# Performance work log

Hardware: AMD Instinct MI355X
Metric: run time of the kernel (lower is better)

Reference implementation:

```python
import jax, jax.numpy as jnp
import numpy as np

A = 2048        # atoms
IN_DEPTH = 128
OUT_DEPTH = 128
FILTER_LEN = 16


def setup_inputs() -> dict:
    key = jax.random.key(0)
    k1, k2, k3, k4 = jax.random.split(key, 4)
    node_property_tensor = jax.random.normal(k1, (A, IN_DEPTH), dtype=jnp.float32)
    connectivity_tensor = jax.random.normal(k2, (A, A, FILTER_LEN), dtype=jnp.float32)
    bond_property_tensor = jax.random.normal(k3, (A, FILTER_LEN, 2), dtype=jnp.float32)
    # filters initialized ~ N(0,1) * 1/in_depth, per the torch init
    filters = jax.random.normal(k4, (OUT_DEPTH, FILTER_LEN, IN_DEPTH + 2), dtype=jnp.float32) / IN_DEPTH
    return {
        "node_property_tensor": node_property_tensor,
        "connectivity_tensor": connectivity_tensor,
        "bond_property_tensor": bond_property_tensor,
        "filters": filters,
    }


def reference(node_property_tensor, connectivity_tensor, bond_property_tensor, filters):
    # gather neighbor features: conn (A,B,F) x node (B,D) -> (A,F,D)
    node_connection = jnp.einsum('abf,bd->afd', connectivity_tensor, node_property_tensor)
    # append bond properties -> (A, F, D+2)
    combined = jnp.concatenate([node_connection, bond_property_tensor], axis=2)
    # fused broadcast-multiply + double-sum: (A,F,K) x (O,F,K) -> (A,O)
    return jnp.einsum('afk,ofk->ao', combined, filters)
```

## Files before the change

### kernel.cpp

```cpp
#include <hip/hip_runtime.h>
#include <stdint.h>

#define N_ATOM 2048
#define K_TOT  32768
#define KCH    2048
#define BK2    128
#define NIT    (KCH / BK2)

typedef __attribute__((ext_vector_type(8))) short bf16x8;
typedef __attribute__((ext_vector_type(4))) float f32x4;

typedef __attribute__((address_space(3))) uint32_t lds_u32;
typedef __attribute__((address_space(1))) uint32_t gbl_u32;

__device__ __forceinline__ void async_ld16(const void* g, void* l) {
  __builtin_amdgcn_global_load_lds((const gbl_u32*)g, (lds_u32*)l, 16, 0, 0);
}

__device__ __forceinline__ unsigned short f2bf(float x) {
  union { float f; uint32_t u; } v; v.f = x;
  uint32_t r = v.u + 0x7FFFu + ((v.u >> 16) & 1u);
  return (unsigned short)(r >> 16);
}

__global__ __launch_bounds__(256) void k_gt(const float* __restrict__ node,
                                            const float* __restrict__ filt,
                                            unsigned short* __restrict__ Gt) {
  __shared__ unsigned short As[128 * 136];
  __shared__ unsigned short Bs[128 * 136];
  const int t  = threadIdx.x;
  const int b0 = blockIdx.x * 128;
  const int n0 = blockIdx.y * 128;

#pragma unroll
  for (int rep = 0; rep < 16; ++rep) {
    int q = rep * 256 + t;
    int row = q >> 5, c4 = q & 31;
    float4 v = *(const float4*)(node + (size_t)(b0 + row) * 128 + c4 * 4);
    unsigned short* dst = &As[row * 136 + c4 * 4];
    dst[0] = f2bf(v.x); dst[1] = f2bf(v.y); dst[2] = f2bf(v.z); dst[3] = f2bf(v.w);
  }
#pragma unroll
  for (int rep = 0; rep < 32; ++rep) {
    int q = rep * 256 + t;
    int row = q >> 6, c2 = q & 63;
    float2 v = *(const float2*)(filt + (size_t)(n0 + row) * 130 + c2 * 2);
    unsigned short* dst = &Bs[row * 136 + c2 * 2];
    dst[0] = f2bf(v.x); dst[1] = f2bf(v.y);
  }
  __syncthreads();

  const int w = t >> 6, l = t & 63;
  const int lm = l & 15, q4 = l >> 4;

  f32x4 acc[2][8];
#pragma unroll
  for (int ms = 0; ms < 2; ++ms)
#pragma unroll
    for (int ns = 0; ns < 8; ++ns)
      acc[ms][ns] = (f32x4){0.f, 0.f, 0.f, 0.f};

#pragma unroll
  for (int ks = 0; ks < 4; ++ks) {
    int ko = ks * 32 + q4 * 8;
    bf16x8 a[2], b[8];
#pragma unroll
    for (int ms = 0; ms < 2; ++ms) {
      int m = w * 32 + ms * 16 + lm;
      a[ms] = *(const bf16x8*)&As[m * 136 + ko];
    }
#pragma unroll
    for (int ns = 0; ns < 8; ++ns) {
      int n = ns * 16 + lm;
      b[ns] = *(const bf16x8*)&Bs[n * 136 + ko];
    }
#pragma unroll
    for (int ms = 0; ms < 2; ++ms)
#pragma unroll
      for (int ns = 0; ns < 8; ++ns)
        acc[ms][ns] = __builtin_amdgcn_mfma_f32_16x16x32_bf16(a[ms], b[ns], acc[ms][ns], 0, 0, 0);
  }

#pragma unroll
  for (int ms = 0; ms < 2; ++ms)
#pragma unroll
    for (int ns = 0; ns < 8; ++ns)
#pragma unroll
      for (int i = 0; i < 4; ++i) {
        int m = w * 32 + ms * 16 + q4 * 4 + i;
        int n = ns * 16 + lm;
        Gt[(size_t)(b0 + m) * 2048 + n0 + n] = f2bf(acc[ms][ns][i]);
      }
}

__global__ __launch_bounds__(256) void k_bond(const float* __restrict__ bond,
                                              const float* __restrict__ filt,
                                              float* __restrict__ out) {
  __shared__ float fb[128 * 32];
  __shared__ float bl[16 * 32];
  const int t  = threadIdx.x;
  const int a0 = blockIdx.x * 16;

#pragma unroll
  for (int r = 0; r < 16; ++r) {
    int idx = r * 256 + t;
    int o = idx >> 5, fj = idx & 31;
    int f = fj >> 1, j = fj & 1;
    fb[idx] = filt[(size_t)o * 2080 + f * 130 + 128 + j];
  }
  bl[t]       = bond[(size_t)a0 * 32 + t];
  bl[256 + t] = bond[(size_t)a0 * 32 + 256 + t];
  __syncthreads();

#pragma unroll
  for (int r = 0; r < 8; ++r) {
    int idx = r * 256 + t;
    int aa = idx >> 7, o = idx & 127;
    const float2* bp = (const float2*)&bl[aa * 32];
    const float2* fp = (const float2*)&fb[o * 32];
    float acc = 0.f;
#pragma unroll
    for (int f = 0; f < 16; ++f) {
      float2 b2 = bp[f], f2 = fp[f];
      acc += b2.x * f2.x + b2.y * f2.y;
    }
    out[(size_t)(a0 + aa) * 128 + o] = acc;
  }
}

__global__ __launch_bounds__(256, 1) void k_main(const float* __restrict__ conn,
                                                 const unsigned short* __restrict__ Gt,
                                                 float* __restrict__ out) {
  __shared__ unsigned short Bh[2][8 * 128 * 16];

  const int t  = threadIdx.x;
  const int w  = t >> 6, l = t & 63;
  const int lm = l & 15, q4 = l >> 4;
  const int a0 = blockIdx.x * 128;
  const int kc = blockIdx.y * KCH;

  f32x4 acc[2][8];
#pragma unroll
  for (int ms = 0; ms < 2; ++ms)
#pragma unroll
    for (int ns = 0; ns < 8; ++ns)
      acc[ms][ns] = (f32x4){0.f, 0.f, 0.f, 0.f};

  const float* arow0 = conn + (size_t)(a0 + w * 32 + lm) * K_TOT;
  const float* arow1 = conn + (size_t)(a0 + w * 32 + 16 + lm) * K_TOT;

  auto stageB = [&](int buf, int k0) {
    const char* gB = (const char*)(Gt + (size_t)k0 * 128);
#pragma unroll
    for (int r = 0; r < 8; ++r) {
      const void* g = gB + (size_t)(r * 256 + t) * 16;
      void* lb = (void*)((char*)&Bh[buf][0] + r * 4096 + w * 1024);
      async_ld16(g, lb);
    }
  };

  float4 Ar[2][4][2];
  auto loadA = [&](int k0) {
#pragma unroll
    for (int kk = 0; kk < 4; ++kk) {
      int off = k0 + kk * 32 + q4 * 8;
      Ar[0][kk][0] = *(const float4*)(arow0 + off);
      Ar[0][kk][1] = *(const float4*)(arow0 + off + 4);
      Ar[1][kk][0] = *(const float4*)(arow1 + off);
      Ar[1][kk][1] = *(const float4*)(arow1 + off + 4);
    }
  };

  stageB(0, kc);
  loadA(kc);
  __syncthreads();

  for (int it = 0; it < NIT; ++it) {
    const int cur = it & 1;

    bf16x8 af[2][4];
#pragma unroll
    for (int ms = 0; ms < 2; ++ms)
#pragma unroll
      for (int kk = 0; kk < 4; ++kk) {
        float4 lo = Ar[ms][kk][0], hi = Ar[ms][kk][1];
        bf16x8 av;
        av[0] = (short)f2bf(lo.x); av[1] = (short)f2bf(lo.y);
        av[2] = (short)f2bf(lo.z); av[3] = (short)f2bf(lo.w);
        av[4] = (short)f2bf(hi.x); av[5] = (short)f2bf(hi.y);
        av[6] = (short)f2bf(hi.z); av[7] = (short)f2bf(hi.w);
        af[ms][kk] = av;
      }

    if (it + 1 < NIT) {
      stageB(1 - cur, kc + (it + 1) * BK2);
      loadA(kc + (it + 1) * BK2);
    }

#pragma unroll
    for (int kk = 0; kk < 4; ++kk) {
      const int b_rel = 2 * kk + (q4 >> 1);
      const int f0 = (q4 & 1) * 8;
      bf16x8 b[8];
#pragma unroll
      for (int ns = 0; ns < 8; ++ns) {
        int o = ns * 16 + lm;
        b[ns] = *(const bf16x8*)&Bh[cur][b_rel * 2048 + o * 16 + f0];
      }
#pragma unroll
      for (int ms = 0; ms < 2; ++ms)
#pragma unroll
        for (int ns = 0; ns < 8; ++ns)
          acc[ms][ns] = __builtin_amdgcn_mfma_f32_16x16x32_bf16(af[ms][kk], b[ns], acc[ms][ns], 0, 0, 0);
    }

    __syncthreads();
  }

#pragma unroll
  for (int ms = 0; ms < 2; ++ms)
#pragma unroll
    for (int ns = 0; ns < 8; ++ns)
#pragma unroll
      for (int i = 0; i < 4; ++i) {
        int m = w * 32 + ms * 16 + q4 * 4 + i;
        int n = ns * 16 + lm;
        atomicAdd(&out[(size_t)(a0 + m) * 128 + n], acc[ms][ns][i]);
      }
}

extern "C" void kernel_launch(void* const* d_in, const int* in_sizes, int n_in,
                              void* d_out, int out_size, void* d_ws, size_t ws_size,
                              hipStream_t stream) {
  const float* node = (const float*)d_in[0];
  const float* conn = (const float*)d_in[1];
  const float* bond = (const float*)d_in[2];
  const float* filt = (const float*)d_in[3];
  float* out = (float*)d_out;

  if (ws_size < (size_t)N_ATOM * 2048 * sizeof(unsigned short)) return;
  unsigned short* Gt = (unsigned short*)d_ws;

  k_gt  <<<dim3(16, 16), 256, 0, stream>>>(node, filt, Gt);
  k_bond<<<dim3(128),    256, 0, stream>>>(bond, filt, out);
  k_main<<<dim3(16, 16), 256, 0, stream>>>(conn, Gt, out);
}
```

Baseline: 430.0 us.

## Double waves per block in main GEMM, halve rows per wave, cheaper bf16 pack

Reorganizes the main GEMM kernel to use 8 waves per block, each owning 16 rows instead of 32, with launch bounds allowing two blocks per CU. This raises the number of waves in flight and lowers per-thread register use, to better hide latency on the streamed connectivity loads. It also switches those loads to nontemporal and replaces per-element bf16 rounding with a pack-and-permute conversion that drops the round-to-even tie term. The trade-off is less B-fragment reuse per LDS read and slightly different rounding.

```diff
diff --git a/kernel.cpp b/kernel.cpp
--- a/kernel.cpp
+++ b/kernel.cpp
@@ -21,6 +21,14 @@
   union { float f; uint32_t u; } v; v.f = x;
   uint32_t r = v.u + 0x7FFFu + ((v.u >> 16) & 1u);
   return (unsigned short)(r >> 16);
+}
+
+__device__ __forceinline__ uint32_t pack_bf2(float x, float y) {
+  union { float f; uint32_t u; } a, b;
+  a.f = x; b.f = y;
+  uint32_t au = a.u + 0x7FFFu;
+  uint32_t bu = b.u + 0x7FFFu;
+  return __builtin_amdgcn_perm(bu, au, 0x07060302u);
 }
 
 __global__ __launch_bounds__(256) void k_gt(const float* __restrict__ node,
@@ -128,7 +136,7 @@
   }
 }
 
-__global__ __launch_bounds__(256, 1) void k_main(const float* __restrict__ conn,
+__global__ __launch_bounds__(512, 2) void k_main(const float* __restrict__ conn,
                                                  const unsigned short* __restrict__ Gt,
                                                  float* __restrict__ out) {
   __shared__ unsigned short Bh[2][8 * 128 * 16];
@@ -139,35 +147,30 @@
   const int a0 = blockIdx.x * 128;
   const int kc = blockIdx.y * KCH;
 
-  f32x4 acc[2][8];
-#pragma unroll
-  for (int ms = 0; ms < 2; ++ms)
-#pragma unroll
-    for (int ns = 0; ns < 8; ++ns)
-      acc[ms][ns] = (f32x4){0.f, 0.f, 0.f, 0.f};
-
-  const float* arow0 = conn + (size_t)(a0 + w * 32 + lm) * K_TOT;
-  const float* arow1 = conn + (size_t)(a0 + w * 32 + 16 + lm) * K_TOT;
+  f32x4 acc[8];
+#pragma unroll
+  for (int ns = 0; ns < 8; ++ns)
+    acc[ns] = (f32x4){0.f, 0.f, 0.f, 0.f};
+
+  const float* arow = conn + (size_t)(a0 + w * 16 + lm) * K_TOT;
 
   auto stageB = [&](int buf, int k0) {
     const char* gB = (const char*)(Gt + (size_t)k0 * 128);
 #pragma unroll
-    for (int r = 0; r < 8; ++r) {
-      const void* g = gB + (size_t)(r * 256 + t) * 16;
-      void* lb = (void*)((char*)&Bh[buf][0] + r * 4096 + w * 1024);
+    for (int r = 0; r < 4; ++r) {
+      const void* g = gB + (size_t)(r * 512 + t) * 16;
+      void* lb = (void*)((char*)&Bh[buf][0] + r * 8192 + w * 1024);
       async_ld16(g, lb);
     }
   };
 
-  float4 Ar[2][4][2];
+  f32x4 Ar[4][2];
   auto loadA = [&](int k0) {
 #pragma unroll
     for (int kk = 0; kk < 4; ++kk) {
-      int off = k0 + kk * 32 + q4 * 8;
-      Ar[0][kk][0] = *(const float4*)(arow0 + off);
-      Ar[0][kk][1] = *(const float4*)(arow0 + off + 4);
-      Ar[1][kk][0] = *(const float4*)(arow1 + off);
-      Ar[1][kk][1] = *(const float4*)(arow1 + off + 4);
+      const float* p = arow + k0 + kk * 32 + q4 * 8;
+      Ar[kk][0] = __builtin_nontemporal_load((const f32x4*)p);
+      Ar[kk][1] = __builtin_nontemporal_load((const f32x4*)(p + 4));
     }
   };
 
@@ -178,19 +181,17 @@
   for (int it = 0; it < NIT; ++it) {
     const int cur = it & 1;
 
-    bf16x8 af[2][4];
-#pragma unroll
-    for (int ms = 0; ms < 2; ++ms)
-#pragma unroll
-      for (int kk = 0; kk < 4; ++kk) {
-        float4 lo = Ar[ms][kk][0], hi = Ar[ms][kk][1];
-        bf16x8 av;
-        av[0] = (short)f2bf(lo.x); av[1] = (short)f2bf(lo.y);
-        av[2] = (short)f2bf(lo.z); av[3] = (short)f2bf(lo.w);
-        av[4] = (short)f2bf(hi.x); av[5] = (short)f2bf(hi.y);
-        av[6] = (short)f2bf(hi.z); av[7] = (short)f2bf(hi.w);
-        af[ms][kk] = av;
-      }
+    bf16x8 af[4];
+#pragma unroll
+    for (int kk = 0; kk < 4; ++kk) {
+      f32x4 lo = Ar[kk][0], hi = Ar[kk][1];
+      union { bf16x8 v; uint32_t u[4]; } cvt;
+      cvt.u[0] = pack_bf2(lo[0], lo[1]);
+      cvt.u[1] = pack_bf2(lo[2], lo[3]);
+      cvt.u[2] = pack_bf2(hi[0], hi[1]);
+      cvt.u[3] = pack_bf2(hi[2], hi[3]);
+      af[kk] = cvt.v;
+    }
 
     if (it + 1 < NIT) {
       stageB(1 - cur, kc + (it + 1) * BK2);
@@ -201,32 +202,25 @@
     for (int kk = 0; kk < 4; ++kk) {
       const int b_rel = 2 * kk + (q4 >> 1);
       const int f0 = (q4 & 1) * 8;
-      bf16x8 b[8];
 #pragma unroll
       for (int ns = 0; ns < 8; ++ns) {
         int o = ns * 16 + lm;
-        b[ns] = *(const bf16x8*)&Bh[cur][b_rel * 2048 + o * 16 + f0];
+        bf16x8 b = *(const bf16x8*)&Bh[cur][b_rel * 2048 + o * 16 + f0];
+        acc[ns] = __builtin_amdgcn_mfma_f32_16x16x32_bf16(af[kk], b, acc[ns], 0, 0, 0);
       }
-#pragma unroll
-      for (int ms = 0; ms < 2; ++ms)
-#pragma unroll
-        for (int ns = 0; ns < 8; ++ns)
-          acc[ms][ns] = __builtin_amdgcn_mfma_f32_16x16x32_bf16(af[ms][kk], b[ns], acc[ms][ns], 0, 0, 0);
     }
 
     __syncthreads();
   }
 
 #pragma unroll
-  for (int ms = 0; ms < 2; ++ms)
-#pragma unroll
-    for (int ns = 0; ns < 8; ++ns)
-#pragma unroll
-      for (int i = 0; i < 4; ++i) {
-        int m = w * 32 + ms * 16 + q4 * 4 + i;
-        int n = ns * 16 + lm;
-        atomicAdd(&out[(size_t)(a0 + m) * 128 + n], acc[ms][ns][i]);
-      }
+  for (int ns = 0; ns < 8; ++ns)
+#pragma unroll
+    for (int i = 0; i < 4; ++i) {
+      int m = w * 16 + q4 * 4 + i;
+      int n = ns * 16 + lm;
+      atomicAdd(&out[(size_t)(a0 + m) * 128 + n], acc[ns][i]);
+    }
 }
 
 extern "C" void kernel_launch(void* const* d_in, const int* in_sizes, int n_in,
@@ -243,5 +237,5 @@
 
   k_gt  <<<dim3(16, 16), 256, 0, stream>>>(node, filt, Gt);
   k_bond<<<dim3(128),    256, 0, stream>>>(bond, filt, out);
-  k_main<<<dim3(16, 16), 256, 0, stream>>>(conn, Gt, out);
-}
+  k_main<<<dim3(16, 16), 512, 0, stream>>>(conn, Gt, out);
+}
```

Result: faster. 417.1 us (-3.0%).
